# Kernel tuning notes

Measured on AMD Instinct MI355X. Metric: run time of the kernel, lower is better.

The kernel has to match this reference:

```python
import jax, jax.numpy as jnp
import numpy as np

B, S, M = 32, 512, 8
DF = 512          # per-feature dim (face/fc/img/label)
DIM1 = 4 * DF     # 2048
DIM2 = 512        # memory dim / hidden dim
EPS = 1e-05


def setup_inputs() -> dict:
    key = jax.random.key(0)
    ks = jax.random.split(key, 10)
    def g(k, shape, scale=1.0):
        return jax.random.normal(k, shape, dtype=jnp.float32) * scale
    fc_feat = g(ks[0], (B, S, DF))
    img_feat = g(ks[1], (B, S, DF))
    label_feat = g(ks[2], (B, DF))
    memory = g(ks[3], (B, M, DIM2))
    face = g(ks[4], (B, S, DF))
    face_mask = jax.random.randint(ks[5], (B, S), 0, 2).astype(jnp.float32)
    # params: linear1 (dim1+dim2 -> dim2) with bias, linear2 (dim2 -> 1) no bias
    xav1 = (2.0 / (DIM1 + DIM2 + DIM2)) ** 0.5
    xav2 = (2.0 / (DIM2 + 1)) ** 0.5
    W1 = g(ks[6], (DIM2, DIM1 + DIM2), xav1)
    b1 = jnp.zeros((DIM2,), dtype=jnp.float32)
    w2 = g(ks[7], (DIM2,), xav2)
    return {"fc_feat": fc_feat, "img_feat": img_feat, "label_feat": label_feat,
            "memory": memory, "face": face, "face_mask": face_mask,
            "W1": W1, "b1": b1, "w2": w2}


def reference(fc_feat, img_feat, label_feat, memory, face, face_mask, W1, b1, w2):
    b, s, _ = face.shape
    m = memory.shape[1]
    # concat along feature dim of (face, fc, img, label) -> [B,S,DIM1]
    base = jnp.concatenate(
        [face, fc_feat, img_feat,
         jnp.broadcast_to(label_feat[:, None, :], (b, s, label_feat.shape[-1]))],
        axis=-1)
    # linear1 split: W1 @ cat(base, mem) = W1a@base + W1b@mem  (avoids B*M*S*(dim1+dim2) concat)
    part_base = jnp.einsum('bsd,hd->bsh', base, W1[:, :DIM1])      # [B,S,H]
    part_mem = jnp.einsum('bmd,hd->bmh', memory, W1[:, DIM1:])     # [B,M,H]
    h = jnp.tanh(part_base[:, None, :, :] + part_mem[:, :, None, :] + b1)  # [B,M,S,H]
    e = jnp.einsum('bmsh,h->bms', h, w2).reshape(b, m * s)         # memory-major flatten
    alpha = jax.nn.softmax(e, axis=1)
    final_mask = jnp.tile(face_mask, (1, m))                       # face_mask.repeat(1, M)
    alpha = alpha * final_mask
    alpha = alpha / (alpha.sum(axis=1, keepdims=True) + EPS)
    # bmm(alpha, face.repeat(1,M,1)) == sum over m,s of alpha * face
    context = jnp.einsum('bms,bsd->bd', alpha.reshape(b, m, s), face)
    return alpha, context
```

## Files before the change

### kernel.cpp

```cpp
#include <hip/hip_runtime.h>
#include <hip/hip_bf16.h>
#include <math.h>

#define NB 32
#define NS 512
#define NM 8
#define NH 512
#define NK 2048
#define WSTRIDE 2560
#define FEPS 1e-5f

typedef __attribute__((ext_vector_type(4))) float f32x4;
typedef __attribute__((ext_vector_type(8))) short bf16x8;
typedef __attribute__((ext_vector_type(8))) unsigned short ushort8;

__device__ __forceinline__ unsigned short f2b(float f) {
  union { __hip_bfloat16 h; unsigned short u; } cv;
  cv.h = __float2bfloat16(f);
  return cv.u;
}

#define LDSK 40

__global__ __launch_bounds__(256, 2)
void gemm_base_kernel(const float* __restrict__ face,
                      const float* __restrict__ fcf,
                      const float* __restrict__ imgf,
                      const float* __restrict__ labf,
                      const float* __restrict__ W1,
                      float* __restrict__ pb)
{
  __shared__ unsigned short As[2][128 * LDSK];
  __shared__ unsigned short Bs[2][128 * LDSK];

  const int tid  = threadIdx.x;
  const int lane = tid & 63;
  const int wid  = tid >> 6;
  const int wr   = wid >> 1;
  const int wc   = wid & 1;
  const int blkm = blockIdx.x >> 2;
  const int blkn = blockIdx.x & 3;

  const int r  = tid >> 1;
  const int ch = (tid & 1) << 4;

  const int gr = blkm * 128 + r;
  const int bb = gr >> 9;
  const int gh = blkn * 128 + r;

  const int rl = lane & 15;
  const int kq = (lane >> 4) << 3;

  f32x4 acc[4][4];
  #pragma unroll
  for (int i = 0; i < 4; ++i)
    #pragma unroll
    for (int j = 0; j < 4; ++j)
      acc[i][j] = (f32x4){0.f, 0.f, 0.f, 0.f};

  float ra[16], rb[16];

#define LOAD_REGS(KT) do {                                                  \
    const int kt_ = (KT);                                                   \
    const int off_ = ((kt_ & 15) << 5) | ch;                                \
    const int reg_ = kt_ >> 4;                                              \
    const float* pa_;                                                       \
    if      (reg_ == 0) pa_ = face + (size_t)gr * 512 + off_;               \
    else if (reg_ == 1) pa_ = fcf  + (size_t)gr * 512 + off_;               \
    else if (reg_ == 2) pa_ = imgf + (size_t)gr * 512 + off_;               \
    else                pa_ = labf + (size_t)bb * 512 + off_;               \
    const float* pw_ = W1 + (size_t)gh * WSTRIDE + (kt_ << 5) + ch;         \
    _Pragma("unroll")                                                       \
    for (int i_ = 0; i_ < 4; ++i_) {                                        \
      f32x4 va_ = *(const f32x4*)(pa_ + 4 * i_);                            \
      f32x4 vb_ = *(const f32x4*)(pw_ + 4 * i_);                            \
      ra[4*i_+0] = va_[0]; ra[4*i_+1] = va_[1];                             \
      ra[4*i_+2] = va_[2]; ra[4*i_+3] = va_[3];                             \
      rb[4*i_+0] = vb_[0]; rb[4*i_+1] = vb_[1];                             \
      rb[4*i_+2] = vb_[2]; rb[4*i_+3] = vb_[3];                             \
    }                                                                       \
  } while (0)

#define WRITE_LDS(BUF) do {                                                 \
    ushort8 a0_, a1_, b0_, b1_;                                             \
    _Pragma("unroll")                                                       \
    for (int j_ = 0; j_ < 8; ++j_) {                                        \
      a0_[j_] = f2b(ra[j_]);   a1_[j_] = f2b(ra[8 + j_]);                   \
      b0_[j_] = f2b(rb[j_]);   b1_[j_] = f2b(rb[8 + j_]);                   \
    }                                                                       \
    *(ushort8*)&As[BUF][r * LDSK + ch]     = a0_;                           \
    *(ushort8*)&As[BUF][r * LDSK + ch + 8] = a1_;                           \
    *(ushort8*)&Bs[BUF][r * LDSK + ch]     = b0_;                           \
    *(ushort8*)&Bs[BUF][r * LDSK + ch + 8] = b1_;                           \
  } while (0)

#define COMPUTE(BUF) do {                                                   \
    bf16x8 af_[4], bf_[4];                                                  \
    _Pragma("unroll")                                                       \
    for (int m_ = 0; m_ < 4; ++m_)                                          \
      af_[m_] = *(const bf16x8*)&As[BUF][(wr*64 + m_*16 + rl) * LDSK + kq]; \
    _Pragma("unroll")                                                       \
    for (int n_ = 0; n_ < 4; ++n_)                                          \
      bf_[n_] = *(const bf16x8*)&Bs[BUF][(wc*64 + n_*16 + rl) * LDSK + kq]; \
    _Pragma("unroll")                                                       \
    for (int m_ = 0; m_ < 4; ++m_)                                          \
      _Pragma("unroll")                                                     \
      for (int n_ = 0; n_ < 4; ++n_)                                        \
        acc[m_][n_] = __builtin_amdgcn_mfma_f32_16x16x32_bf16(              \
            af_[m_], bf_[n_], acc[m_][n_], 0, 0, 0);                        \
  } while (0)

  LOAD_REGS(0);
  WRITE_LDS(0);
  __syncthreads();

  int buf = 0;
  for (int kt = 0; kt < 64; ++kt) {
    if (kt < 63) LOAD_REGS(kt + 1);
    COMPUTE(buf);
    if (kt < 63) WRITE_LDS(buf ^ 1);
    __syncthreads();
    buf ^= 1;
  }

  const int crow = blkm * 128 + wr * 64;
  const int ccol = blkn * 128 + wc * 64 + rl;
  #pragma unroll
  for (int m = 0; m < 4; ++m)
    #pragma unroll
    for (int n = 0; n < 4; ++n)
      #pragma unroll
      for (int j = 0; j < 4; ++j) {
        const int row = crow + m * 16 + (lane >> 4) * 4 + j;
        pb[(size_t)row * 512 + ccol + n * 16] = acc[m][n][j];
      }

#undef LOAD_REGS
#undef WRITE_LDS
#undef COMPUTE
}

__global__ __launch_bounds__(256)
void pm_kernel(const float* __restrict__ memory,
               const float* __restrict__ W1,
               const float* __restrict__ b1,
               float* __restrict__ pm)
{
  __shared__ float ms[NM * 512];
  const int b = blockIdx.x;
  const int t = threadIdx.x;

  const float* src = memory + (size_t)b * NM * 512;
  #pragma unroll
  for (int i = 0; i < 4; ++i)
    ((f32x4*)ms)[t + i * 256] = ((const f32x4*)src)[t + i * 256];
  __syncthreads();

  #pragma unroll
  for (int hh = 0; hh < 2; ++hh) {
    const int h = t + hh * 256;
    const float* wrow = W1 + (size_t)h * WSTRIDE + 2048;
    float acc[NM];
    #pragma unroll
    for (int m = 0; m < NM; ++m) acc[m] = 0.f;
    for (int d = 0; d < 512; d += 4) {
      f32x4 w = *(const f32x4*)(wrow + d);
      #pragma unroll
      for (int m = 0; m < NM; ++m) {
        f32x4 mv = *(const f32x4*)&ms[m * 512 + d];
        acc[m] += w[0]*mv[0] + w[1]*mv[1] + w[2]*mv[2] + w[3]*mv[3];
      }
    }
    const float bias = b1[h];
    #pragma unroll
    for (int m = 0; m < NM; ++m)
      pm[((size_t)b * NM + m) * 512 + h] = acc[m] + bias;
  }
}

__global__ __launch_bounds__(128)
void e_kernel(const float* __restrict__ pb,
              const float* __restrict__ pm,
              const float* __restrict__ w2,
              float* __restrict__ e)
{
  __shared__ float pbs[16 * 516];
  __shared__ float pms[NM * 516];
  __shared__ float w2s[512];

  const int b  = blockIdx.x;
  const int st = blockIdx.y;
  const int t  = threadIdx.x;

  const float* pbsrc = pb + ((size_t)b * NS + st * 16) * 512;
  #pragma unroll
  for (int i = 0; i < 16; ++i) {
    const int fi = t + i * 128;
    f32x4 v = ((const f32x4*)pbsrc)[fi];
    const int f32i = fi * 4;
    *(f32x4*)&pbs[(f32i >> 9) * 516 + (f32i & 511)] = v;
  }
  const float* pmsrc = pm + (size_t)b * NM * 512;
  #pragma unroll
  for (int i = 0; i < 8; ++i) {
    const int fi = t + i * 128;
    f32x4 v = ((const f32x4*)pmsrc)[fi];
    const int f32i = fi * 4;
    *(f32x4*)&pms[(f32i >> 9) * 516 + (f32i & 511)] = v;
  }
  ((f32x4*)w2s)[t] = ((const f32x4*)w2)[t];
  __syncthreads();

  const int sl = t >> 3;
  const int m  = t & 7;
  const float* prow = &pbs[sl * 516];
  const float* mrow = &pms[m * 516];

  float acc = 0.f;
  for (int h = 0; h < 512; h += 4) {
    f32x4 pv = *(const f32x4*)&prow[h];
    f32x4 mv = *(const f32x4*)&mrow[h];
    f32x4 wv = *(const f32x4*)&w2s[h];
    #pragma unroll
    for (int j = 0; j < 4; ++j) {
      const float x  = pv[j] + mv[j];
      const float ex = __expf(x + x);
      const float th = 1.f - __fdividef(2.f, ex + 1.f);
      acc += wv[j] * th;
    }
  }
  e[(size_t)b * (NM * NS) + m * NS + st * 16 + sl] = acc;
}

__global__ __launch_bounds__(256)
void softmax_ctx_kernel(const float* __restrict__ e,
                        const float* __restrict__ face,
                        const float* __restrict__ face_mask,
                        float* __restrict__ out_alpha,
                        float* __restrict__ out_ctx)
{
  __shared__ float ev[NM * NS];
  __shared__ float msk[NS];
  __shared__ float ws[NS];
  __shared__ float redX[4], redA[4], redM[4];

  const int b = blockIdx.x;
  const int t = threadIdx.x;
  const int lane = t & 63;
  const int wv = t >> 6;

  const float* erow = e + (size_t)b * (NM * NS);
  #pragma unroll
  for (int i = 0; i < 4; ++i)
    ((f32x4*)ev)[t + i * 256] = ((const f32x4*)erow)[t + i * 256];
  if (t < 128)
    ((f32x4*)msk)[t] = ((const f32x4*)(face_mask + (size_t)b * NS))[t];
  __syncthreads();

  float mx = -3.402823466e38f;
  for (int i = t; i < NM * NS; i += 256) mx = fmaxf(mx, ev[i]);
  #pragma unroll
  for (int o = 32; o >= 1; o >>= 1) mx = fmaxf(mx, __shfl_xor(mx, o));
  if (lane == 0) redX[wv] = mx;
  __syncthreads();
  mx = fmaxf(fmaxf(redX[0], redX[1]), fmaxf(redX[2], redX[3]));

  float sA = 0.f, sM = 0.f;
  for (int i = t; i < NM * NS; i += 256) {
    const float p = __expf(ev[i] - mx);
    ev[i] = p;
    sA += p;
    sM += p * msk[i & 511];
  }
  #pragma unroll
  for (int o = 32; o >= 1; o >>= 1) {
    sA += __shfl_xor(sA, o);
    sM += __shfl_xor(sM, o);
  }
  if (lane == 0) { redA[wv] = sA; redM[wv] = sM; }
  __syncthreads();
  sA = redA[0] + redA[1] + redA[2] + redA[3];
  sM = redM[0] + redM[1] + redM[2] + redM[3];

  const float rr = sM / sA;
  const float scale = 1.f / (sA * (rr + FEPS));

  for (int i = t; i < NM * NS; i += 256) {
    const float a = ev[i] * msk[i & 511] * scale;
    ev[i] = a;
    out_alpha[(size_t)b * (NM * NS) + i] = a;
  }
  __syncthreads();

  for (int s = t; s < NS; s += 256) {
    float w = 0.f;
    #pragma unroll
    for (int m = 0; m < NM; ++m) w += ev[m * NS + s];
    ws[s] = w;
  }
  __syncthreads();

  const float* fb = face + (size_t)b * NS * 512;
  for (int d = t; d < 512; d += 256) {
    float c = 0.f;
    for (int s = 0; s < NS; ++s) c += ws[s] * fb[(size_t)s * 512 + d];
    out_ctx[(size_t)b * 512 + d] = c;
  }
}

extern "C" void kernel_launch(void* const* d_in, const int* in_sizes, int n_in,
                              void* d_out, int out_size, void* d_ws, size_t ws_size,
                              hipStream_t stream)
{
  const float* fc_feat  = (const float*)d_in[0];
  const float* img_feat = (const float*)d_in[1];
  const float* label    = (const float*)d_in[2];
  const float* memory   = (const float*)d_in[3];
  const float* face     = (const float*)d_in[4];
  const float* fmask    = (const float*)d_in[5];
  const float* W1       = (const float*)d_in[6];
  const float* b1       = (const float*)d_in[7];
  const float* w2       = (const float*)d_in[8];

  float* out       = (float*)d_out;
  float* alpha_out = out;
  float* ctx_out   = out + (size_t)NB * NM * NS;

  char* ws = (char*)d_ws;
  float* pb = (float*)ws;
  float* pm = (float*)(ws + (size_t)NB * NS * 512 * 4);
  float* ee = (float*)(ws + (size_t)NB * NS * 512 * 4
                          + (size_t)NB * NM * 512 * 4);

  gemm_base_kernel<<<512, 256, 0, stream>>>(face, fc_feat, img_feat, label, W1, pb);
  pm_kernel<<<NB, 256, 0, stream>>>(memory, W1, b1, pm);
  e_kernel<<<dim3(NB, NS / 16), 128, 0, stream>>>(pb, pm, w2, ee);
  softmax_ctx_kernel<<<NB, 256, 0, stream>>>(ee, face, fmask, alpha_out, ctx_out);
}
```

Baseline: 353.2 us.

## Split-K the base GEMM, parallelize pm and context kernels across more blocks

The base GEMM is split into two K halves across 1024 blocks with an XCD-aware block remap, writing two partial buffers that e_kernel sums when loading. pm_kernel now spreads hidden rows over a second grid dimension and uses wave-level shuffle reductions. The context reduction moves out of the softmax kernel into a separate ctx_kernel that splits S across blocks and accumulates with atomics after a memset. Together these target the low occupancy of the serial per-batch tails and the small GEMM grid, at the cost of an extra pb buffer of traffic, more launches, and atomics.

```diff
diff --git a/kernel.cpp b/kernel.cpp
--- a/kernel.cpp
+++ b/kernel.cpp
@@ -6,7 +6,6 @@
 #define NS 512
 #define NM 8
 #define NH 512
-#define NK 2048
 #define WSTRIDE 2560
 #define FEPS 1e-5f
 
@@ -22,7 +21,8 @@
 
 #define LDSK 40
 
-__global__ __launch_bounds__(256, 2)
+template<int KSTEPS>
+__global__ __launch_bounds__(256, 4)
 void gemm_base_kernel(const float* __restrict__ face,
                       const float* __restrict__ fcf,
                       const float* __restrict__ imgf,
@@ -38,8 +38,13 @@
   const int wid  = tid >> 6;
   const int wr   = wid >> 1;
   const int wc   = wid & 1;
-  const int blkm = blockIdx.x >> 2;
-  const int blkn = blockIdx.x & 3;
+
+  const int bid = blockIdx.x;
+  const int cpx = gridDim.x >> 3;
+  const int sid = (bid & 7) * cpx + (bid >> 3);
+  const int kk   = sid >> 9;
+  const int blkm = (sid >> 2) & 127;
+  const int blkn = sid & 3;
 
   const int r  = tid >> 1;
   const int ch = (tid & 1) << 4;
@@ -60,8 +65,8 @@
 
   float ra[16], rb[16];
 
-#define LOAD_REGS(KT) do {                                                  \
-    const int kt_ = (KT);                                                   \
+#define LOAD_REGS(KTG) do {                                                 \
+    const int kt_ = (KTG);                                                  \
     const int off_ = ((kt_ & 15) << 5) | ch;                                \
     const int reg_ = kt_ >> 4;                                              \
     const float* pa_;                                                       \
@@ -110,19 +115,22 @@
             af_[m_], bf_[n_], acc[m_][n_], 0, 0, 0);                        \
   } while (0)
 
-  LOAD_REGS(0);
+  const int kbase = kk * 32;
+  LOAD_REGS(kbase);
   WRITE_LDS(0);
   __syncthreads();
 
   int buf = 0;
-  for (int kt = 0; kt < 64; ++kt) {
-    if (kt < 63) LOAD_REGS(kt + 1);
+  #pragma unroll 1
+  for (int kt = 0; kt < KSTEPS; ++kt) {
+    if (kt < KSTEPS - 1) LOAD_REGS(kbase + kt + 1);
     COMPUTE(buf);
-    if (kt < 63) WRITE_LDS(buf ^ 1);
+    if (kt < KSTEPS - 1) WRITE_LDS(buf ^ 1);
     __syncthreads();
     buf ^= 1;
   }
 
+  float* pbo = pb + (size_t)kk * ((size_t)NB * NS * 512);
   const int crow = blkm * 128 + wr * 64;
   const int ccol = blkn * 128 + wc * 64 + rl;
   #pragma unroll
@@ -132,7 +140,7 @@
       #pragma unroll
       for (int j = 0; j < 4; ++j) {
         const int row = crow + m * 16 + (lane >> 4) * 4 + j;
-        pb[(size_t)row * 512 + ccol + n * 16] = acc[m][n][j];
+        pbo[(size_t)row * 512 + ccol + n * 16] = acc[m][n][j];
       }
 
 #undef LOAD_REGS
@@ -147,8 +155,11 @@
                float* __restrict__ pm)
 {
   __shared__ float ms[NM * 512];
-  const int b = blockIdx.x;
-  const int t = threadIdx.x;
+  const int b  = blockIdx.x;
+  const int ht = blockIdx.y;
+  const int t  = threadIdx.x;
+  const int w  = t >> 6;
+  const int l  = t & 63;
 
   const float* src = memory + (size_t)b * NM * 512;
   #pragma unroll
@@ -156,30 +167,38 @@
     ((f32x4*)ms)[t + i * 256] = ((const f32x4*)src)[t + i * 256];
   __syncthreads();
 
-  #pragma unroll
-  for (int hh = 0; hh < 2; ++hh) {
-    const int h = t + hh * 256;
+  #pragma unroll 1
+  for (int i = 0; i < 16; ++i) {
+    const int h = ht * 64 + w * 16 + i;
     const float* wrow = W1 + (size_t)h * WSTRIDE + 2048;
-    float acc[NM];
-    #pragma unroll
-    for (int m = 0; m < NM; ++m) acc[m] = 0.f;
-    for (int d = 0; d < 512; d += 4) {
-      f32x4 w = *(const f32x4*)(wrow + d);
+    const f32x4 w0 = *(const f32x4*)(wrow + l * 4);
+    const f32x4 w1 = *(const f32x4*)(wrow + 256 + l * 4);
+    float part[NM];
+    #pragma unroll
+    for (int m = 0; m < NM; ++m) {
+      const f32x4 m0 = *(const f32x4*)&ms[m * 512 + l * 4];
+      const f32x4 m1 = *(const f32x4*)&ms[m * 512 + 256 + l * 4];
+      part[m] = w0[0]*m0[0] + w0[1]*m0[1] + w0[2]*m0[2] + w0[3]*m0[3]
+              + w1[0]*m1[0] + w1[1]*m1[1] + w1[2]*m1[2] + w1[3]*m1[3];
+    }
+    #pragma unroll
+    for (int off = 32; off >= 1; off >>= 1)
       #pragma unroll
-      for (int m = 0; m < NM; ++m) {
-        f32x4 mv = *(const f32x4*)&ms[m * 512 + d];
-        acc[m] += w[0]*mv[0] + w[1]*mv[1] + w[2]*mv[2] + w[3]*mv[3];
-      }
+      for (int m = 0; m < NM; ++m)
+        part[m] += __shfl_xor(part[m], off);
+    if (l == 0) {
+      const float bias = b1[h];
+      #pragma unroll
+      for (int m = 0; m < NM; ++m)
+        pm[((size_t)b * NM + m) * 512 + h] = part[m] + bias;
     }
-    const float bias = b1[h];
-    #pragma unroll
-    for (int m = 0; m < NM; ++m)
-      pm[((size_t)b * NM + m) * 512 + h] = acc[m] + bias;
-  }
-}
-
+  }
+}
+
+template<int SPLIT>
 __global__ __launch_bounds__(128)
-void e_kernel(const float* __restrict__ pb,
+void e_kernel(const float* __restrict__ pb0,
+              const float* __restrict__ pb1,
               const float* __restrict__ pm,
               const float* __restrict__ w2,
               float* __restrict__ e)
@@ -192,11 +211,16 @@
   const int st = blockIdx.y;
   const int t  = threadIdx.x;
 
-  const float* pbsrc = pb + ((size_t)b * NS + st * 16) * 512;
+  const f32x4* s0 = (const f32x4*)(pb0 + ((size_t)b * NS + st * 16) * 512);
+  const f32x4* s1 = (const f32x4*)(pb1 + ((size_t)b * NS + st * 16) * 512);
   #pragma unroll
   for (int i = 0; i < 16; ++i) {
     const int fi = t + i * 128;
-    f32x4 v = ((const f32x4*)pbsrc)[fi];
+    f32x4 v = s0[fi];
+    if (SPLIT) {
+      f32x4 v1 = s1[fi];
+      v[0]+=v1[0]; v[1]+=v1[1]; v[2]+=v1[2]; v[3]+=v1[3];
+    }
     const int f32i = fi * 4;
     *(f32x4*)&pbs[(f32i >> 9) * 516 + (f32i & 511)] = v;
   }
@@ -233,15 +257,13 @@
 }
 
 __global__ __launch_bounds__(256)
-void softmax_ctx_kernel(const float* __restrict__ e,
-                        const float* __restrict__ face,
-                        const float* __restrict__ face_mask,
-                        float* __restrict__ out_alpha,
-                        float* __restrict__ out_ctx)
+void softmax_kernel(const float* __restrict__ e,
+                    const float* __restrict__ face_mask,
+                    float* __restrict__ out_alpha,
+                    float* __restrict__ wsum)
 {
   __shared__ float ev[NM * NS];
   __shared__ float msk[NS];
-  __shared__ float ws[NS];
   __shared__ float redX[4], redA[4], redM[4];
 
   const int b = blockIdx.x;
@@ -296,16 +318,34 @@
     float w = 0.f;
     #pragma unroll
     for (int m = 0; m < NM; ++m) w += ev[m * NS + s];
-    ws[s] = w;
-  }
-  __syncthreads();
-
-  const float* fb = face + (size_t)b * NS * 512;
-  for (int d = t; d < 512; d += 256) {
-    float c = 0.f;
-    for (int s = 0; s < NS; ++s) c += ws[s] * fb[(size_t)s * 512 + d];
-    out_ctx[(size_t)b * 512 + d] = c;
-  }
+    wsum[(size_t)b * NS + s] = w;
+  }
+}
+
+__global__ __launch_bounds__(128)
+void ctx_kernel(const float* __restrict__ wsum,
+                const float* __restrict__ face,
+                float* __restrict__ out_ctx)
+{
+  const int b  = blockIdx.x;
+  const int sq = blockIdx.y;
+  const int t  = threadIdx.x;
+
+  f32x4 acc = (f32x4){0.f, 0.f, 0.f, 0.f};
+  const int s0 = sq * 64;
+  #pragma unroll 4
+  for (int si = 0; si < 64; ++si) {
+    const int s = s0 + si;
+    const float w = wsum[(size_t)b * NS + s];
+    const f32x4 fv = ((const f32x4*)(face + ((size_t)b * NS + s) * 512))[t];
+    acc[0] += w * fv[0]; acc[1] += w * fv[1];
+    acc[2] += w * fv[2]; acc[3] += w * fv[3];
+  }
+  float* dst = out_ctx + (size_t)b * 512 + t * 4;
+  atomicAdd(dst + 0, acc[0]);
+  atomicAdd(dst + 1, acc[1]);
+  atomicAdd(dst + 2, acc[2]);
+  atomicAdd(dst + 3, acc[3]);
 }
 
 extern "C" void kernel_launch(void* const* d_in, const int* in_sizes, int n_in,
@@ -326,14 +366,34 @@
   float* alpha_out = out;
   float* ctx_out   = out + (size_t)NB * NM * NS;
 
+  const size_t szPB = (size_t)NB * NS * 512 * 4;
+  const size_t szPM = (size_t)NB * NM * 512 * 4;
+  const size_t szE  = (size_t)NB * NM * NS * 4;
+  const size_t need_split = 2 * szPB + szPM + szE + (size_t)NB * NS * 4;
+  const bool split = ws_size >= need_split;
+
   char* ws = (char*)d_ws;
-  float* pb = (float*)ws;
-  float* pm = (float*)(ws + (size_t)NB * NS * 512 * 4);
-  float* ee = (float*)(ws + (size_t)NB * NS * 512 * 4
-                          + (size_t)NB * NM * 512 * 4);
-
-  gemm_base_kernel<<<512, 256, 0, stream>>>(face, fc_feat, img_feat, label, W1, pb);
-  pm_kernel<<<NB, 256, 0, stream>>>(memory, W1, b1, pm);
-  e_kernel<<<dim3(NB, NS / 16), 128, 0, stream>>>(pb, pm, w2, ee);
-  softmax_ctx_kernel<<<NB, 256, 0, stream>>>(ee, face, fmask, alpha_out, ctx_out);
-}
+  float* pb0 = (float*)ws;
+  float* pb1 = split ? (float*)(ws + szPB) : pb0;
+  char*  tail = ws + (split ? 2 * szPB : szPB);
+  float* pm = (float*)tail;
+  float* ee = (float*)(tail + szPM);
+  float* wsum = (float*)(tail + szPM + szE);
+
+  hipMemsetAsync(ctx_out, 0, (size_t)NB * 512 * 4, stream);
+
+  if (split)
+    gemm_base_kernel<32><<<1024, 256, 0, stream>>>(face, fc_feat, img_feat, label, W1, pb0);
+  else
+    gemm_base_kernel<64><<<512, 256, 0, stream>>>(face, fc_feat, img_feat, label, W1, pb0);
+
+  pm_kernel<<<dim3(NB, 8), 256, 0, stream>>>(memory, W1, b1, pm);
+
+  if (split)
+    e_kernel<1><<<dim3(NB, NS / 16), 128, 0, stream>>>(pb0, pb1, pm, w2, ee);
+  else
+    e_kernel<0><<<dim3(NB, NS / 16), 128, 0, stream>>>(pb0, pb1, pm, w2, ee);
+
+  softmax_kernel<<<NB, 256, 0, stream>>>(ee, fmask, alpha_out, wsum);
+  ctx_kernel<<<dim3(NB, 8), 128, 0, stream>>>(wsum, face, ctx_out);
+}
```

New measurement: 330.7 us. -6.4%, faster.
